# Kernel optimization log

Hardware: AMD Instinct MI355X
Metric: run time of the kernel (lower is better)

Reference implementation:

```python
import jax, jax.numpy as jnp
import numpy as np

N, E, F_IN, H, C = 50000, 800000, 256, 128, 40


def _gcn_norm(edge_index, num_nodes, dtype):
    # add self loops (fill value 1.0), symmetric normalization D^-1/2 A D^-1/2
    src, dst = edge_index[0], edge_index[1]
    loop = jnp.arange(num_nodes, dtype=src.dtype)
    src = jnp.concatenate([src, loop])
    dst = jnp.concatenate([dst, loop])
    w = jnp.ones(src.shape[0], dtype=dtype)
    deg = jax.ops.segment_sum(w, dst, num_segments=num_nodes)
    dinv = jnp.where(deg > 0, jax.lax.rsqrt(deg), jnp.zeros_like(deg))
    norm = dinv[src] * w * dinv[dst]
    return src, dst, norm


def _propagate(x, src, dst, w, num_nodes):
    # gather x[src], scale by edge weight, scatter-add at dst (SpMM)
    return jax.ops.segment_sum(w[:, None] * x[src], dst, num_segments=num_nodes)


def _mixhop_conv(x, src, dst, w, Ws, b):
    # powers = [0, 1, 2]; Ws[p] is [in, out]
    n = x.shape[0]
    outs = [x @ Ws[0]]
    h = x
    for p in (1, 2):
        h = _propagate(h, src, dst, w, n)
        outs.append(h @ Ws[p])
    return jnp.concatenate(outs, axis=-1) + b


def setup_inputs() -> dict:
    key = jax.random.key(0)
    ks = jax.random.split(key, 10)
    x = jax.random.normal(ks[0], (N, F_IN), dtype=jnp.float32)
    edge_index = jax.random.randint(ks[1], (2, E), 0, N, dtype=jnp.int64)
    s1 = 1.0 / np.sqrt(F_IN)
    s2 = 1.0 / np.sqrt(3 * H)
    return {
        "x": x,
        "edge_index": edge_index,
        "W1_0": jax.random.uniform(ks[2], (F_IN, H), jnp.float32, -s1, s1),
        "W1_1": jax.random.uniform(ks[3], (F_IN, H), jnp.float32, -s1, s1),
        "W1_2": jax.random.uniform(ks[4], (F_IN, H), jnp.float32, -s1, s1),
        "b1": jnp.zeros((3 * H,), jnp.float32),
        "W2_0": jax.random.uniform(ks[5], (3 * H, C), jnp.float32, -s2, s2),
        "W2_1": jax.random.uniform(ks[6], (3 * H, C), jnp.float32, -s2, s2),
        "W2_2": jax.random.uniform(ks[7], (3 * H, C), jnp.float32, -s2, s2),
        "b2": jnp.zeros((3 * C,), jnp.float32),
    }


def reference(x, edge_index, W1_0, W1_1, W1_2, b1, W2_0, W2_1, W2_2, b2):
    n = x.shape[0]
    src, dst, w = _gcn_norm(edge_index, n, x.dtype)
    h = jax.nn.relu(_mixhop_conv(x, src, dst, w, (W1_0, W1_1, W1_2), b1))
    # eval mode: dropout is identity
    out = _mixhop_conv(h, src, dst, w, (W2_0, W2_1, W2_2), b2)
    return jax.nn.log_softmax(out, axis=1)
```

## Files before the change

kernel.cpp:

```cpp
#include <hip/hip_runtime.h>
#include <hip/hip_bf16.h>
#include <math.h>

#define N_NODES 50000
#define F_IN 256
#define H1 128
#define C_OUT 40
#define L1W 384
#define L2W 120
#define L2WP 128
#define NBUK 196
#define NBLK1 256

typedef __attribute__((ext_vector_type(8))) short short8;
typedef __attribute__((ext_vector_type(4))) float f32x4;
typedef __attribute__((ext_vector_type(2))) float f32x2;
typedef __attribute__((ext_vector_type(4))) unsigned short us4;

__device__ inline unsigned short f2bf(float f) {
    union { float f; unsigned int u; } x;
    x.f = f;
    unsigned int u = x.u;
    return (unsigned short)((u + 0x7FFF + ((u >> 16) & 1)) >> 16);
}
__device__ inline float bf2f(unsigned short u) {
    union { unsigned int u; float f; } x;
    x.u = (unsigned int)u << 16;
    return x.f;
}
__device__ inline unsigned int pack_fp8x4(float a, float b, float c, float d) {
    int v = 0;
    v = __builtin_amdgcn_cvt_pk_fp8_f32(a, b, v, false);
    v = __builtin_amdgcn_cvt_pk_fp8_f32(c, d, v, true);
    return (unsigned int)v;
}
__device__ inline unsigned char pack_fp8x1(float a) {
    return (unsigned char)(__builtin_amdgcn_cvt_pk_fp8_f32(a, a, 0, false) & 0xFF);
}
#define EDGE_S(r) ((int)((r) & 0xFFFFu))
#define EDGE_W(r) bf2f((unsigned short)((r) >> 16))


__global__ void detect_k(const int* __restrict__ ei, int* __restrict__ flag) {
    __shared__ int any;
    if (threadIdx.x == 0) any = 0;
    __syncthreads();
    int v = 0;
    for (int r = 0; r < 4; r++) {
        int e = threadIdx.x + r * 256;
        v |= ei[e * 2 + 1];
    }
    if (v != 0) atomicOr(&any, 1);
    __syncthreads();
    if (threadIdx.x == 0) *flag = any;
}


__global__ void hist_k(const int* __restrict__ ei, const int* __restrict__ flag,
                       int* __restrict__ cnt, int E) {
    int base = (blockIdx.x * 256 + threadIdx.x) * 4;
    if (base >= E) return;
    if (base + 4 <= E) {
        int d0, d1, d2, d3;
        if (*flag) {
            int4 dv = *(const int4*)(ei + E + base);
            d0 = dv.x; d1 = dv.y; d2 = dv.z; d3 = dv.w;
        } else {
            const long long* e64 = (const long long*)ei;
            longlong2 a = *(const longlong2*)(e64 + E + base);
            longlong2 b = *(const longlong2*)(e64 + E + base + 2);
            d0 = (int)a.x; d1 = (int)a.y; d2 = (int)b.x; d3 = (int)b.y;
        }
        atomicAdd(&cnt[d0], 1);
        atomicAdd(&cnt[d1], 1);
        atomicAdd(&cnt[d2], 1);
        atomicAdd(&cnt[d3], 1);
    } else {
        for (int e = base; e < E; e++) {
            int d = (*flag) ? ei[E + e] : (int)((const long long*)ei)[E + e];
            atomicAdd(&cnt[d], 1);
        }
    }
}


__global__ __launch_bounds__(256) void scan1_k(const int* __restrict__ cnt,
                                               int* __restrict__ bsum, int n) {
    int t = threadIdx.x;
    int i = blockIdx.x * 256 + t;
    int v = (i < n) ? cnt[i] : 0;
    for (int off = 32; off; off >>= 1) v += __shfl_down(v, off, 64);
    __shared__ int ws[4];
    if ((t & 63) == 0) ws[t >> 6] = v;
    __syncthreads();
    if (t == 0) bsum[blockIdx.x] = ws[0] + ws[1] + ws[2] + ws[3];
}

__global__ __launch_bounds__(256) void scan2_k(int* __restrict__ bsum,
                                               int* __restrict__ btot, int nb) {
    __shared__ int s[256];
    int t = threadIdx.x;
    int v = (t < nb) ? bsum[t] : 0;
    s[t] = v;
    __syncthreads();
    for (int off = 1; off < 256; off <<= 1) {
        int u = (t >= off) ? s[t - off] : 0;
        __syncthreads();
        s[t] += u;
        __syncthreads();
    }
    if (t < nb) bsum[t] = s[t] - v;
    if (t == nb - 1) *btot = s[t];
}

__global__ __launch_bounds__(256) void scan3_k(const int* __restrict__ cnt,
                                               const int* __restrict__ bsum,
                                               int* __restrict__ rowptr,
                                               float* __restrict__ dinv, int n) {
    __shared__ int s[256];
    int t = threadIdx.x;
    int i = blockIdx.x * 256 + t;
    int v = (i < n) ? cnt[i] : 0;
    s[t] = v;
    __syncthreads();
    for (int off = 1; off < 256; off <<= 1) {
        int u = (t >= off) ? s[t - off] : 0;
        __syncthreads();
        s[t] += u;
        __syncthreads();
    }
    if (i < n) {
        rowptr[i] = s[t] - v + bsum[blockIdx.x];
        if (dinv) dinv[i] = rsqrtf((float)v + 1.0f);
    }
}


__global__ __launch_bounds__(256) void hist2_k(const int* __restrict__ ei,
                                               const int* __restrict__ flag,
                                               int* __restrict__ cnt2, int E) {
    __shared__ int lcnt[NBUK];
    int t = threadIdx.x, blk = blockIdx.x;
    for (int j = t; j < NBUK; j += 256) lcnt[j] = 0;
    __syncthreads();
    int chunk = (E + NBLK1 - 1) / NBLK1;
    int beg = blk * chunk, end = min(beg + chunk, E);
    bool i32 = (*flag) != 0;
    const long long* e64 = (const long long*)ei;
    for (int e = beg + t; e < end; e += 256) {
        int d = i32 ? ei[E + e] : (int)e64[E + e];
        atomicAdd(&lcnt[d >> 8], 1);
    }
    __syncthreads();
    for (int j = t; j < NBUK; j += 256) cnt2[j * NBLK1 + blk] = lcnt[j];
}

__global__ __launch_bounds__(256) void stage_k(const int* __restrict__ ei,
                                               const int* __restrict__ flag,
                                               const int* __restrict__ off2,
                                               unsigned int* __restrict__ stage, int E) {
    __shared__ int lcur[NBUK];
    int t = threadIdx.x, blk = blockIdx.x;
    for (int j = t; j < NBUK; j += 256) lcur[j] = off2[j * NBLK1 + blk];
    __syncthreads();
    int chunk = (E + NBLK1 - 1) / NBLK1;
    int beg = blk * chunk, end = min(beg + chunk, E);
    bool i32 = (*flag) != 0;
    const long long* e64 = (const long long*)ei;
    for (int e = beg + t; e < end; e += 256) {
        int s, d;
        if (i32) { s = ei[e]; d = ei[E + e]; }
        else { s = (int)e64[e]; d = (int)e64[E + e]; }
        int b = d >> 8;
        int pos = atomicAdd(&lcur[b], 1);
        stage[pos] = ((unsigned int)(d & 255) << 16) | (unsigned int)s;
    }
}

__global__ __launch_bounds__(256) void scatter2_k(const unsigned int* __restrict__ stage,
                                                  const int* __restrict__ off2,
                                                  const int* __restrict__ rowptr,
                                                  const float* __restrict__ dinv,
                                                  unsigned int* __restrict__ csr,
                                                  int E, int n) {
    __shared__ int lfill[256];
    int b = blockIdx.x, t = threadIdx.x;
    int node0 = b << 8;
    int node = node0 + t;
    lfill[t] = (node < n) ? rowptr[node] : 0;
    __syncthreads();
    int segBeg = off2[b * NBLK1];
    int segEnd = (b == NBUK - 1) ? E : off2[(b + 1) * NBLK1];
    for (int e = segBeg + t; e < segEnd; e += 256) {
        unsigned int rec = stage[e];
        int dl = rec >> 16;
        int s = rec & 0xFFFF;
        int d = node0 + dl;
        float w = dinv[s] * dinv[d];
        int pos = atomicAdd(&lfill[dl], 1);
        csr[pos] = ((unsigned int)f2bf(w) << 16) | (unsigned int)s;
    }
}


#define N1PACK ((F_IN / 32) * L1W * 32)
#define N2PACK ((L1W / 32) * L2WP * 32)

__global__ void pack_k(const float* __restrict__ w10, const float* __restrict__ w11,
                       const float* __restrict__ w12, const float* __restrict__ w20,
                       const float* __restrict__ w21, const float* __restrict__ w22,
                       unsigned short* __restrict__ Bp1, unsigned short* __restrict__ Bp2) {
    int idx = blockIdx.x * 256 + threadIdx.x;
    if (idx < N1PACK) {
        int kk = idx & 31;
        int nn = (idx >> 5) % L1W;
        int kt = idx / (L1W * 32);
        int k = kt * 32 + kk;
        int p = nn >> 7, c = nn & 127;
        const float* w = (p == 0) ? w10 : (p == 1) ? w11 : w12;
        Bp1[idx] = f2bf(w[k * H1 + c]);
    } else if (idx < N1PACK + N2PACK) {
        int j = idx - N1PACK;
        int kk = j & 31;
        int nn = (j >> 5) & (L2WP - 1);
        int kt = j >> 12;
        int k = kt * 32 + kk;
        unsigned short v = 0;
        if (nn < L2W) {
            int p = nn / 40, c = nn % 40;
            const float* w = (p == 0) ? w20 : (p == 1) ? w21 : w22;
            v = f2bf(w[k * C_OUT + c]);
        }
        Bp2[j] = v;
    }
}


__global__ __launch_bounds__(256, 3) void mgemm1_k(const float* __restrict__ A,
                                                   const unsigned short* __restrict__ Bp,
                                                   const float* __restrict__ b1,
                                                   unsigned short* __restrict__ Hb,
                                                   unsigned char* __restrict__ Y8, int N) {
    __shared__ unsigned short Bs[2][L1W * 32];
    int tid = threadIdx.x;
    int wave = tid >> 6, lane = tid & 63;
    int m = lane & 15, kq = lane >> 4;
    int row0 = blockIdx.x * 64 + wave * 16;
    int arow = row0 + m;
    if (arow >= N) arow = N - 1;
    const float* Ap = A + (size_t)arow * F_IN + kq * 8;

    f32x4 acc[24];
#pragma unroll
    for (int s = 0; s < 24; s++) acc[s] = (f32x4){0.f, 0.f, 0.f, 0.f};

    short8 breg[6];
    float4 af0, af1;
#pragma unroll
    for (int c = 0; c < 6; c++) {
        int t = tid + c * 256;
        breg[c] = *(const short8*)(Bp + (size_t)t * 8);
    }
    af0 = *(const float4*)(Ap);
    af1 = *(const float4*)(Ap + 4);
#pragma unroll
    for (int c = 0; c < 6; c++) {
        int t = tid + c * 256;
        int col = t >> 2, pp = t & 3;
        *(short8*)(&Bs[0][col * 32 + ((pp ^ ((col >> 1) & 3)) << 3)]) = breg[c];
    }
    __syncthreads();

    for (int kt = 0; kt < F_IN / 32; kt++) {
        short8 a;
        a[0] = (short)f2bf(af0.x); a[1] = (short)f2bf(af0.y);
        a[2] = (short)f2bf(af0.z); a[3] = (short)f2bf(af0.w);
        a[4] = (short)f2bf(af1.x); a[5] = (short)f2bf(af1.y);
        a[6] = (short)f2bf(af1.z); a[7] = (short)f2bf(af1.w);
        if (kt < F_IN / 32 - 1) {
            const unsigned short* Bn = Bp + (size_t)(kt + 1) * L1W * 32;
#pragma unroll
            for (int c = 0; c < 6; c++) {
                int t = tid + c * 256;
                breg[c] = *(const short8*)(Bn + (size_t)t * 8);
            }
            af0 = *(const float4*)(Ap + (kt + 1) * 32);
            af1 = *(const float4*)(Ap + (kt + 1) * 32 + 4);
        }
        const unsigned short* Bbuf = Bs[kt & 1];
#pragma unroll
        for (int s = 0; s < 24; s++) {
            int col = s * 16 + m;
            short8 b = *(const short8*)(&Bbuf[col * 32 + ((kq ^ ((col >> 1) & 3)) << 3)]);
            acc[s] = __builtin_amdgcn_mfma_f32_16x16x32_bf16(a, b, acc[s], 0, 0, 0);
        }
        if (kt < F_IN / 32 - 1) {
            int nb = (kt + 1) & 1;
#pragma unroll
            for (int c = 0; c < 6; c++) {
                int t = tid + c * 256;
                int col = t >> 2, pp = t & 3;
                *(short8*)(&Bs[nb][col * 32 + ((pp ^ ((col >> 1) & 3)) << 3)]) = breg[c];
            }
        }
        __syncthreads();
    }
    int crow = row0 + kq * 4;
#pragma unroll
    for (int s = 0; s < 8; s++) {
        int col = s * 16 + m;
        float bias = b1[col];
#pragma unroll
        for (int r = 0; r < 4; r++) {
            int row = crow + r;
            if (row < N) Hb[(size_t)row * L1W + col] = f2bf(fmaxf(acc[s][r] + bias, 0.f));
        }
    }
#pragma unroll
    for (int r = 0; r < 4; r++) {
        int row = crow + r;
        if (row < N) {
            uint4 u;
            u.x = pack_fp8x4(acc[8][r], acc[9][r], acc[10][r], acc[11][r]);
            u.y = pack_fp8x4(acc[12][r], acc[13][r], acc[14][r], acc[15][r]);
            u.z = pack_fp8x4(acc[16][r], acc[17][r], acc[18][r], acc[19][r]);
            u.w = pack_fp8x4(acc[20][r], acc[21][r], acc[22][r], acc[23][r]);
            *(uint4*)(Y8 + (size_t)row * 256 + m * 16) = u;
        }
    }
}


__global__ __launch_bounds__(256) void mgemm2_k(const unsigned short* __restrict__ A,
                                                const unsigned short* __restrict__ Bp,
                                                unsigned short* __restrict__ Ub,
                                                unsigned char* __restrict__ U8, int N) {
    __shared__ unsigned short Bs[2][L2WP * 32];
    int tid = threadIdx.x;
    int wave = tid >> 6, lane = tid & 63;
    int m = lane & 15, kq = lane >> 4;
    int row0 = blockIdx.x * 64 + wave * 16;
    int arow = row0 + m;
    if (arow >= N) arow = N - 1;
    const unsigned short* Ap = A + (size_t)arow * L1W + kq * 8;

    f32x4 acc[8];
#pragma unroll
    for (int s = 0; s < 8; s++) acc[s] = (f32x4){0.f, 0.f, 0.f, 0.f};

    short8 breg[2];
    short8 areg;
#pragma unroll
    for (int c = 0; c < 2; c++) {
        int t = tid + c * 256;
        breg[c] = *(const short8*)(Bp + (size_t)t * 8);
    }
    areg = *(const short8*)(Ap);
#pragma unroll
    for (int c = 0; c < 2; c++) {
        int t = tid + c * 256;
        int col = t >> 2, pp = t & 3;
        *(short8*)(&Bs[0][col * 32 + ((pp ^ ((col >> 1) & 3)) << 3)]) = breg[c];
    }
    __syncthreads();

    for (int kt = 0; kt < L1W / 32; kt++) {
        short8 a = areg;
        if (kt < L1W / 32 - 1) {
            const unsigned short* Bn = Bp + (size_t)(kt + 1) * L2WP * 32;
#pragma unroll
            for (int c = 0; c < 2; c++) {
                int t = tid + c * 256;
                breg[c] = *(const short8*)(Bn + (size_t)t * 8);
            }
            areg = *(const short8*)(Ap + (kt + 1) * 32);
        }
        const unsigned short* Bbuf = Bs[kt & 1];
#pragma unroll
        for (int s = 0; s < 8; s++) {
            int col = s * 16 + m;
            short8 b = *(const short8*)(&Bbuf[col * 32 + ((kq ^ ((col >> 1) & 3)) << 3)]);
            acc[s] = __builtin_amdgcn_mfma_f32_16x16x32_bf16(a, b, acc[s], 0, 0, 0);
        }
        if (kt < L1W / 32 - 1) {
            int nb = (kt + 1) & 1;
#pragma unroll
            for (int c = 0; c < 2; c++) {
                int t = tid + c * 256;
                int col = t >> 2, pp = t & 3;
                *(short8*)(&Bs[nb][col * 32 + ((pp ^ ((col >> 1) & 3)) << 3)]) = breg[c];
            }
        }
        __syncthreads();
    }
    int crow = row0 + kq * 4;
#pragma unroll
    for (int s = 0; s < 3; s++) {
        int col = s * 16 + m;
#pragma unroll
        for (int r = 0; r < 4; r++) {
            int row = crow + r;
            if (row < N) Ub[(size_t)row * L2WP + col] = f2bf(acc[s][r]);
        }
    }
#pragma unroll
    for (int r = 0; r < 4; r++) {
        int row = crow + r;
        if (row < N) {
            uint2 u;
            u.x = pack_fp8x4(acc[0][r], acc[1][r], acc[2][r], acc[3][r]);
            u.y = pack_fp8x4(acc[4][r], acc[5][r], acc[6][r], acc[7][r]);
            *(uint2*)(U8 + (size_t)row * 128 + m * 8) = u;
        }
    }
}


__global__ __launch_bounds__(256) void prop256f_k(const unsigned char* __restrict__ Y8,
                                                  unsigned short* __restrict__ Hb,
                                                  unsigned char* __restrict__ T8,
                                                  const int* __restrict__ rowptr,
                                                  const unsigned int* __restrict__ csr,
                                                  const float* __restrict__ dinv,
                                                  const float* __restrict__ b1, int n) {
    int wave = threadIdx.x >> 6, lane = threadIdx.x & 63;
    int i = blockIdx.x * 4 + wave;
    if (i >= n) return;
    int beg = rowptr[i], end = rowptr[i + 1];
    float di = dinv[i];
    const unsigned int* sbase = (const unsigned int*)Y8 + lane;
    unsigned int sv = sbase[(size_t)i * 64];
    float w = di * di;
    f32x2 slo = __builtin_amdgcn_cvt_pk_f32_fp8(sv, false);
    f32x2 shi = __builtin_amdgcn_cvt_pk_f32_fp8(sv, true);
    float a0 = w * slo.x, a1 = w * slo.y, a2 = w * shi.x, a3 = w * shi.y;

#define CONS256(rr, vv)                                                       \
    _Pragma("unroll") for (int e = 0; e < 8; e++) {                           \
        float we = EDGE_W(rr[e]);                                             \
        f32x2 lo = __builtin_amdgcn_cvt_pk_f32_fp8(vv[e], false);             \
        f32x2 hi = __builtin_amdgcn_cvt_pk_f32_fp8(vv[e], true);              \
        a0 = fmaf(we, lo.x, a0);                                              \
        a1 = fmaf(we, lo.y, a1);                                              \
        a2 = fmaf(we, hi.x, a2);                                              \
        a3 = fmaf(we, hi.y, a3);                                              \
    }

    int nfull = (end - beg) >> 3;
    unsigned int rrA[8], rrB[8];
    if (nfull > 0) {
#pragma unroll
        for (int e = 0; e < 8; e++) rrA[e] = csr[beg + e];
        int it = 0;
        while (it + 2 <= nfull) {
            {
                unsigned int vv[8];
#pragma unroll
                for (int e = 0; e < 8; e++) vv[e] = sbase[(size_t)EDGE_S(rrA[e]) * 64];
#pragma unroll
                for (int e = 0; e < 8; e++) rrB[e] = csr[beg + ((it + 1) << 3) + e];
                CONS256(rrA, vv)
            }
            {
                unsigned int vv[8];
#pragma unroll
                for (int e = 0; e < 8; e++) vv[e] = sbase[(size_t)EDGE_S(rrB[e]) * 64];
                if (it + 2 < nfull) {
#pragma unroll
                    for (int e = 0; e < 8; e++) rrA[e] = csr[beg + ((it + 2) << 3) + e];
                }
                CONS256(rrB, vv)
            }
            it += 2;
        }
        if (it < nfull) {
            unsigned int vv[8];
#pragma unroll
            for (int e = 0; e < 8; e++) vv[e] = sbase[(size_t)EDGE_S(rrA[e]) * 64];
            CONS256(rrA, vv)
        }
    }
    int k = beg + (nfull << 3);
    if (k < end) {
        unsigned int rrt[8];
#pragma unroll
        for (int e = 0; e < 8; e++) {
            int idx = k + e;
            rrt[e] = csr[idx < end ? idx : beg];
        }
        unsigned int vv[8];
#pragma unroll
        for (int e = 0; e < 8; e++) vv[e] = sbase[(size_t)EDGE_S(rrt[e]) * 64];
#pragma unroll
        for (int e = 0; e < 8; e++) {
            float we = (k + e < end) ? EDGE_W(rrt[e]) : 0.f;
            f32x2 lo = __builtin_amdgcn_cvt_pk_f32_fp8(vv[e], false);
            f32x2 hi = __builtin_amdgcn_cvt_pk_f32_fp8(vv[e], true);
            a0 = fmaf(we, lo.x, a0);
            a1 = fmaf(we, lo.y, a1);
            a2 = fmaf(we, hi.x, a2);
            a3 = fmaf(we, hi.y, a3);
        }
    }
#undef CONS256
    int m = lane >> 2, jj = lane & 3;
    if (jj < 2) {
        float av[4] = {a0, a1, a2, a3};
#pragma unroll
        for (int j = 0; j < 4; j++) {
            int L = (4 * jj + j) * 16 + m;
            Hb[(size_t)i * L1W + 128 + L] = f2bf(fmaxf(av[j] + b1[128 + L], 0.f));
        }
    } else {
        unsigned int o = pack_fp8x4(a0, a1, a2, a3);
        *(unsigned int*)(T8 + (size_t)i * 128 + m * 8 + 4 * (jj - 2)) = o;
    }
}


__global__ __launch_bounds__(256) void prop128f_k(const unsigned char* __restrict__ T8,
                                                  unsigned short* __restrict__ Hb,
                                                  const int* __restrict__ rowptr,
                                                  const unsigned int* __restrict__ csr,
                                                  const float* __restrict__ dinv,
                                                  const float* __restrict__ b1, int n) {
    int wave = threadIdx.x >> 6, lane = threadIdx.x & 63;
    int i = blockIdx.x * 4 + wave;
    if (i >= n) return;
    int beg = rowptr[i], end = rowptr[i + 1];
    float di = dinv[i];
    const unsigned short* sbase = (const unsigned short*)T8 + lane;
    unsigned int sv = sbase[(size_t)i * 64];
    float w = di * di;
    f32x2 sd = __builtin_amdgcn_cvt_pk_f32_fp8(sv, false);
    float a0 = w * sd.x, a1 = w * sd.y;

#define CONS128(rr, vv)                                                       \
    _Pragma("unroll") for (int e = 0; e < 8; e++) {                           \
        float we = EDGE_W(rr[e]);                                             \
        f32x2 d = __builtin_amdgcn_cvt_pk_f32_fp8(vv[e], false);              \
        a0 = fmaf(we, d.x, a0);                                               \
        a1 = fmaf(we, d.y, a1);                                               \
    }

    int nfull = (end - beg) >> 3;
    unsigned int rrA[8], rrB[8];
    if (nfull > 0) {
#pragma unroll
        for (int e = 0; e < 8; e++) rrA[e] = csr[beg + e];
        int it = 0;
        while (it + 2 <= nfull) {
            {
                unsigned int vv[8];
#pragma unroll
                for (int e = 0; e < 8; e++) vv[e] = sbase[(size_t)EDGE_S(rrA[e]) * 64];
#pragma unroll
                for (int e = 0; e < 8; e++) rrB[e] = csr[beg + ((it + 1) << 3) + e];
                CONS128(rrA, vv)
            }
            {
                unsigned int vv[8];
#pragma unroll
                for (int e = 0; e < 8; e++) vv[e] = sbase[(size_t)EDGE_S(rrB[e]) * 64];
                if (it + 2 < nfull) {
#pragma unroll
                    for (int e = 0; e < 8; e++) rrA[e] = csr[beg + ((it + 2) << 3) + e];
                }
                CONS128(rrB, vv)
            }
            it += 2;
        }
        if (it < nfull) {
            unsigned int vv[8];
#pragma unroll
            for (int e = 0; e < 8; e++) vv[e] = sbase[(size_t)EDGE_S(rrA[e]) * 64];
            CONS128(rrA, vv)
        }
    }
    int k = beg + (nfull << 3);
    if (k < end) {
        unsigned int rrt[8];
#pragma unroll
        for (int e = 0; e < 8; e++) {
            int idx = k + e;
            rrt[e] = csr[idx < end ? idx : beg];
        }
        unsigned int vv[8];
#pragma unroll
        for (int e = 0; e < 8; e++) vv[e] = sbase[(size_t)EDGE_S(rrt[e]) * 64];
#pragma unroll
        for (int e = 0; e < 8; e++) {
            float we = (k + e < end) ? EDGE_W(rrt[e]) : 0.f;
            f32x2 d = __builtin_amdgcn_cvt_pk_f32_fp8(vv[e], false);
            a0 = fmaf(we, d.x, a0);
            a1 = fmaf(we, d.y, a1);
        }
    }
#undef CONS128
    int m = lane >> 2, u0 = (2 * lane) & 7;
    int L0 = u0 * 16 + m, L1 = (u0 + 1) * 16 + m;
    Hb[(size_t)i * L1W + 256 + L0] = f2bf(fmaxf(a0 + b1[256 + L0], 0.f));
    Hb[(size_t)i * L1W + 256 + L1] = f2bf(fmaxf(a1 + b1[256 + L1], 0.f));
}


__global__ __launch_bounds__(256) void propU8_k(const unsigned char* __restrict__ U8,
                                                unsigned short* __restrict__ T2a,
                                                unsigned char* __restrict__ T8b,
                                                const int* __restrict__ rowptr,
                                                const unsigned int* __restrict__ csr,
                                                const float* __restrict__ dinv, int n) {
    int wave = threadIdx.x >> 6, lane = threadIdx.x & 63;
    int i = blockIdx.x * 4 + wave;
    if (i >= n) return;
    int beg = rowptr[i], end = rowptr[i + 1];
    float di = dinv[i];
    int g = lane >> 5, c = lane & 31;
    const unsigned int* sbase = (const unsigned int*)U8 + c;
    float a0 = 0.f, a1 = 0.f, a2 = 0.f, a3 = 0.f;
    if (g == 0) {
        unsigned int sv = sbase[(size_t)i * 32];
        float w = di * di;
        f32x2 lo = __builtin_amdgcn_cvt_pk_f32_fp8(sv, false);
        f32x2 hi = __builtin_amdgcn_cvt_pk_f32_fp8(sv, true);
        a0 = w * lo.x; a1 = w * lo.y; a2 = w * hi.x; a3 = w * hi.y;
    }

#define CONSU8(rr, vv)                                                        \
    _Pragma("unroll") for (int j = 0; j < 4; j++) {                           \
        float we = EDGE_W(rr[j]);                                             \
        f32x2 lo = __builtin_amdgcn_cvt_pk_f32_fp8(vv[j], false);             \
        f32x2 hi = __builtin_amdgcn_cvt_pk_f32_fp8(vv[j], true);              \
        a0 = fmaf(we, lo.x, a0);                                              \
        a1 = fmaf(we, lo.y, a1);                                              \
        a2 = fmaf(we, hi.x, a2);                                              \
        a3 = fmaf(we, hi.y, a3);                                              \
    }

    int k0 = beg + g;
    int cnt = (k0 < end) ? ((end - k0 + 1) >> 1) : 0;
    int nfull = cnt >> 2;
    unsigned int rrA[4], rrB[4];
    if (nfull > 0) {
#pragma unroll
        for (int j = 0; j < 4; j++) rrA[j] = csr[k0 + 2 * j];
        int it = 0;
        while (it + 2 <= nfull) {
            {
                unsigned int vv[4];
#pragma unroll
                for (int j = 0; j < 4; j++) vv[j] = sbase[(size_t)EDGE_S(rrA[j]) * 32];
#pragma unroll
                for (int j = 0; j < 4; j++) rrB[j] = csr[k0 + ((it + 1) << 3) + 2 * j];
                CONSU8(rrA, vv)
            }
            {
                unsigned int vv[4];
#pragma unroll
                for (int j = 0; j < 4; j++) vv[j] = sbase[(size_t)EDGE_S(rrB[j]) * 32];
                if (it + 2 < nfull) {
#pragma unroll
                    for (int j = 0; j < 4; j++) rrA[j] = csr[k0 + ((it + 2) << 3) + 2 * j];
                }
                CONSU8(rrB, vv)
            }
            it += 2;
        }
        if (it < nfull) {
            unsigned int vv[4];
#pragma unroll
            for (int j = 0; j < 4; j++) vv[j] = sbase[(size_t)EDGE_S(rrA[j]) * 32];
            CONSU8(rrA, vv)
        }
    }
    int t0 = nfull << 2;
    if (t0 < cnt) {
        unsigned int rrt[4], vv[4];
#pragma unroll
        for (int j = 0; j < 4; j++) {
            int t = t0 + j;
            rrt[j] = csr[t < cnt ? k0 + 2 * t : beg];
        }
#pragma unroll
        for (int j = 0; j < 4; j++) vv[j] = sbase[(size_t)EDGE_S(rrt[j]) * 32];
#pragma unroll
        for (int j = 0; j < 4; j++) {
            float we = (t0 + j < cnt) ? EDGE_W(rrt[j]) : 0.f;
            f32x2 lo = __builtin_amdgcn_cvt_pk_f32_fp8(vv[j], false);
            f32x2 hi = __builtin_amdgcn_cvt_pk_f32_fp8(vv[j], true);
            a0 = fmaf(we, lo.x, a0);
            a1 = fmaf(we, lo.y, a1);
            a2 = fmaf(we, hi.x, a2);
            a3 = fmaf(we, hi.y, a3);
        }
    }
#undef CONSU8
    a0 += __shfl_xor(a0, 32, 64);
    a1 += __shfl_xor(a1, 32, 64);
    a2 += __shfl_xor(a2, 32, 64);
    a3 += __shfl_xor(a3, 32, 64);
    if (lane < 32) {
        int m = lane >> 1, sb = 4 * (lane & 1);
        float av[4] = {a0, a1, a2, a3};
#pragma unroll
        for (int j = 0; j < 4; j++) {
            int L = (sb + j) * 16 + m;
            if (L >= 40 && L < 80) T2a[(size_t)i * 40 + (L - 40)] = f2bf(av[j]);
            else if (L >= 80 && L < 120) T8b[(size_t)i * 40 + (L - 80)] = pack_fp8x1(av[j]);
        }
    }
}


__global__ __launch_bounds__(256) void lsm_prop_k(const unsigned short* __restrict__ Ub,
                                                  const unsigned short* __restrict__ T2a,
                                                  const unsigned char* __restrict__ T8b,
                                                  const int* __restrict__ rowptr,
                                                  const unsigned int* __restrict__ csr,
                                                  const float* __restrict__ dinv,
                                                  const float* __restrict__ b2,
                                                  float* __restrict__ out, int n) {
    int wave = threadIdx.x >> 6;
    int lane = threadIdx.x & 63;
    int i = blockIdx.x * 4 + wave;
    if (i >= n) return;
    int beg = rowptr[i], end = rowptr[i + 1];
    float di = dinv[i];
    int g = lane / 10;
    int c = lane - g * 10;
    bool act = lane < 60;
    const unsigned int* sb = (const unsigned int*)T8b + c;
    float a0 = 0.f, a1 = 0.f, a2 = 0.f, a3 = 0.f;
    if (lane < 10) {
        unsigned int sv = sb[(size_t)i * 10];
        float w = di * di;
        f32x2 lo = __builtin_amdgcn_cvt_pk_f32_fp8(sv, false);
        f32x2 hi = __builtin_amdgcn_cvt_pk_f32_fp8(sv, true);
        a0 = w * lo.x; a1 = w * lo.y; a2 = w * hi.x; a3 = w * hi.y;
    }

#define CONSLS(rr, vv)                                                        \
    _Pragma("unroll") for (int j = 0; j < 4; j++) {                           \
        float we = EDGE_W(rr[j]);                                             \
        f32x2 lo = __builtin_amdgcn_cvt_pk_f32_fp8(vv[j], false);             \
        f32x2 hi = __builtin_amdgcn_cvt_pk_f32_fp8(vv[j], true);              \
        a0 = fmaf(we, lo.x, a0);                                              \
        a1 = fmaf(we, lo.y, a1);                                              \
        a2 = fmaf(we, hi.x, a2);                                              \
        a3 = fmaf(we, hi.y, a3);                                              \
    }

    int k0 = beg + g;
    int cnt = (act && k0 < end) ? ((end - k0 + 5) / 6) : 0;
    int nfull = cnt >> 2;
    unsigned int rrA[4], rrB[4];
    if (nfull > 0) {
#pragma unroll
        for (int j = 0; j < 4; j++) rrA[j] = csr[k0 + 6 * j];
        int it = 0;
        while (it + 2 <= nfull) {
            {
                unsigned int vv[4];
#pragma unroll
                for (int j = 0; j < 4; j++) vv[j] = sb[(size_t)EDGE_S(rrA[j]) * 10];
#pragma unroll
                for (int j = 0; j < 4; j++) rrB[j] = csr[k0 + (it + 1) * 24 + 6 * j];
                CONSLS(rrA, vv)
            }
            {
                unsigned int vv[4];
#pragma unroll
                for (int j = 0; j < 4; j++) vv[j] = sb[(size_t)EDGE_S(rrB[j]) * 10];
                if (it + 2 < nfull) {
#pragma unroll
                    for (int j = 0; j < 4; j++) rrA[j] = csr[k0 + (it + 2) * 24 + 6 * j];
                }
                CONSLS(rrB, vv)
            }
            it += 2;
        }
        if (it < nfull) {
            unsigned int vv[4];
#pragma unroll
            for (int j = 0; j < 4; j++) vv[j] = sb[(size_t)EDGE_S(rrA[j]) * 10];
            CONSLS(rrA, vv)
        }
    }
    int t0 = nfull << 2;
    if (t0 < cnt) {
        unsigned int rrt[4], vv[4];
#pragma unroll
        for (int j = 0; j < 4; j++) {
            int t = t0 + j;
            rrt[j] = csr[t < cnt ? k0 + 6 * t : beg];
        }
#pragma unroll
        for (int j = 0; j < 4; j++) vv[j] = sb[(size_t)EDGE_S(rrt[j]) * 10];
#pragma unroll
        for (int j = 0; j < 4; j++) {
            float we = (t0 + j < cnt) ? EDGE_W(rrt[j]) : 0.f;
            f32x2 lo = __builtin_amdgcn_cvt_pk_f32_fp8(vv[j], false);
            f32x2 hi = __builtin_amdgcn_cvt_pk_f32_fp8(vv[j], true);
            a0 = fmaf(we, lo.x, a0);
            a1 = fmaf(we, lo.y, a1);
            a2 = fmaf(we, hi.x, a2);
            a3 = fmaf(we, hi.y, a3);
        }
    }
#undef CONSLS
    float r0s = a0, r1s = a1, r2s = a2, r3s = a3;
#pragma unroll
    for (int g2 = 1; g2 < 6; g2++) {
        r0s += __shfl(a0, lane + 10 * g2, 64);
        r1s += __shfl(a1, lane + 10 * g2, 64);
        r2s += __shfl(a2, lane + 10 * g2, 64);
        r3s += __shfl(a3, lane + 10 * g2, 64);
    }
    int j1 = lane + 64;
    int idx = j1 - 80;
    int srcl = (idx < 0) ? 0 : (idx >> 2);
    float s0v = __shfl(r0s, srcl, 64);
    float s1v = __shfl(r1s, srcl, 64);
    float s2v = __shfl(r2s, srcl, 64);
    float s3v = __shfl(r3s, srcl, 64);
    int comp = idx & 3;
    float pv = (comp == 0) ? s0v : (comp == 1) ? s1v : (comp == 2) ? s2v : s3v;
    float v0, v1;
    {
        int j = lane;
        float v = (j >= 40) ? bf2f(T2a[(size_t)i * 40 + (j - 40)]) : bf2f(Ub[(size_t)i * L2WP + j]);
        v0 = v + b2[j];
    }
    if (j1 < 120) {
        float v = (j1 < 80) ? bf2f(T2a[(size_t)i * 40 + (j1 - 40)]) : pv;
        v1 = v + b2[j1];
    } else {
        v1 = -INFINITY;
    }
    float m = fmaxf(v0, v1);
    for (int off = 32; off; off >>= 1) m = fmaxf(m, __shfl_xor(m, off, 64));
    float s = expf(v0 - m) + ((j1 < 120) ? expf(v1 - m) : 0.f);
    for (int off = 32; off; off >>= 1) s += __shfl_xor(s, off, 64);
    float ls = logf(s) + m;
    out[(size_t)i * 120 + lane] = v0 - ls;
    if (j1 < 120) out[(size_t)i * 120 + j1] = v1 - ls;
}


static inline size_t align256(size_t x) { return (x + 255) & ~(size_t)255; }

extern "C" void kernel_launch(void* const* d_in, const int* in_sizes, int n_in,
                              void* d_out, int out_size, void* d_ws, size_t ws_size,
                              hipStream_t stream) {
    const float* x = (const float*)d_in[0];
    const int* ei = (const int*)d_in[1];
    const float* W1_0 = (const float*)d_in[2];
    const float* W1_1 = (const float*)d_in[3];
    const float* W1_2 = (const float*)d_in[4];
    const float* b1 = (const float*)d_in[5];
    const float* W2_0 = (const float*)d_in[6];
    const float* W2_1 = (const float*)d_in[7];
    const float* W2_2 = (const float*)d_in[8];
    const float* b2 = (const float*)d_in[9];
    float* out = (float*)d_out;

    const int n = N_NODES;
    const int E = in_sizes[1] / 2;
    const int nb = (n + 255) / 256;
    const int nbe4 = ((E + 3) / 4 + 255) / 256;
    const int n2 = NBUK * NBLK1;
    const int nb2 = (n2 + 255) / 256;

    char* p = (char*)d_ws;
    size_t off = 0;
    auto alloc = [&](size_t bytes) {
        void* r = p + off;
        off = align256(off + bytes);
        return r;
    };
    int* flag = (int*)alloc(4);
    int* cnt = (int*)alloc((size_t)n * 4);
    int* rowptr = (int*)alloc((size_t)(n + 1) * 4);
    int* bsum = (int*)alloc((size_t)nb * 4);
    float* dinv = (float*)alloc((size_t)n * 4);
    unsigned int* csr = (unsigned int*)alloc((size_t)E * 4);
    int* cnt2 = (int*)alloc((size_t)n2 * 4);
    int* off2 = (int*)alloc((size_t)n2 * 4);
    int* bsum2 = (int*)alloc((size_t)nb2 * 4);
    int* tot2 = (int*)alloc(4);
    unsigned int* stage = (unsigned int*)alloc((size_t)E * 4);
    unsigned short* Bp1 = (unsigned short*)alloc((size_t)N1PACK * 2);
    unsigned short* Bp2 = (unsigned short*)alloc((size_t)N2PACK * 2);
    unsigned short* Hb = (unsigned short*)alloc((size_t)n * L1W * 2);
    unsigned char* Y8 = (unsigned char*)alloc((size_t)n * 256);
    unsigned char* T8 = (unsigned char*)alloc((size_t)n * 128);
    unsigned short* Ub = (unsigned short*)alloc((size_t)n * L2WP * 2);
    unsigned char* U8 = (unsigned char*)alloc((size_t)n * 128);
    unsigned short* T2a = (unsigned short*)alloc((size_t)n * C_OUT * 2);
    unsigned char* T8b = (unsigned char*)alloc((size_t)n * C_OUT);
    (void)ws_size;

    detect_k<<<1, 256, 0, stream>>>(ei, flag);

    hipMemsetAsync(cnt, 0, (size_t)n * 4, stream);
    hist_k<<<nbe4, 256, 0, stream>>>(ei, flag, cnt, E);
    scan1_k<<<nb, 256, 0, stream>>>(cnt, bsum, n);
    scan2_k<<<1, 256, 0, stream>>>(bsum, rowptr + n, nb);
    scan3_k<<<nb, 256, 0, stream>>>(cnt, bsum, rowptr, dinv, n);

    hist2_k<<<NBLK1, 256, 0, stream>>>(ei, flag, cnt2, E);
    scan1_k<<<nb2, 256, 0, stream>>>(cnt2, bsum2, n2);
    scan2_k<<<1, 256, 0, stream>>>(bsum2, tot2, nb2);
    scan3_k<<<nb2, 256, 0, stream>>>(cnt2, bsum2, off2, (float*)nullptr, n2);
    stage_k<<<NBLK1, 256, 0, stream>>>(ei, flag, off2, stage, E);
    scatter2_k<<<NBUK, 256, 0, stream>>>(stage, off2, rowptr, dinv, csr, E, n);

    pack_k<<<(N1PACK + N2PACK + 255) / 256, 256, 0, stream>>>(W1_0, W1_1, W1_2,
                                                              W2_0, W2_1, W2_2, Bp1, Bp2);

    mgemm1_k<<<(n + 63) / 64, 256, 0, stream>>>(x, Bp1, b1, Hb, Y8, n);
    prop256f_k<<<(n + 3) / 4, 256, 0, stream>>>(Y8, Hb, T8, rowptr, csr, dinv, b1, n);
    prop128f_k<<<(n + 3) / 4, 256, 0, stream>>>(T8, Hb, rowptr, csr, dinv, b1, n);

    mgemm2_k<<<(n + 63) / 64, 256, 0, stream>>>(Hb, Bp2, Ub, U8, n);
    propU8_k<<<(n + 3) / 4, 256, 0, stream>>>(U8, T2a, T8b, rowptr, csr, dinv, n);

    lsm_prop_k<<<(n + 3) / 4, 256, 0, stream>>>(Ub, T2a, T8b, rowptr, csr, dinv, b2, out, n);
}
```

Before: 346.1 us.

## Split first GEMM across two column halves per row tile

The layer-1 GEMM now launches two blocks per 64-row tile, each computing 192 of the 384 output columns. This halves the accumulator registers and shared memory per block, allowing occupancy to go from 3 to 4 blocks per CU and doubling the grid for more parallelism. The cost is that each block reloads and converts the same fp32 A rows, doubling A reads and conversions. The epilogue is split so each half writes its portion of the bf16 and fp8 outputs.

```diff
diff --git a/kernel.cpp b/kernel.cpp
--- a/kernel.cpp
+++ b/kernel.cpp
@@ -236,35 +236,38 @@
 }
 
 
-__global__ __launch_bounds__(256, 3) void mgemm1_k(const float* __restrict__ A,
+__global__ __launch_bounds__(256, 4) void mgemm1_k(const float* __restrict__ A,
                                                    const unsigned short* __restrict__ Bp,
                                                    const float* __restrict__ b1,
                                                    unsigned short* __restrict__ Hb,
                                                    unsigned char* __restrict__ Y8, int N) {
-    __shared__ unsigned short Bs[2][L1W * 32];
+    __shared__ unsigned short Bs[2][192 * 32];
     int tid = threadIdx.x;
     int wave = tid >> 6, lane = tid & 63;
     int m = lane & 15, kq = lane >> 4;
-    int row0 = blockIdx.x * 64 + wave * 16;
+    int blkM = blockIdx.x >> 1, blkN = blockIdx.x & 1;
+    int s0 = blkN * 12;
+    int row0 = blkM * 64 + wave * 16;
     int arow = row0 + m;
     if (arow >= N) arow = N - 1;
     const float* Ap = A + (size_t)arow * F_IN + kq * 8;
-
-    f32x4 acc[24];
-#pragma unroll
-    for (int s = 0; s < 24; s++) acc[s] = (f32x4){0.f, 0.f, 0.f, 0.f};
-
-    short8 breg[6];
+    const unsigned short* Bp0 = Bp + (size_t)s0 * 16 * 32;
+
+    f32x4 acc[12];
+#pragma unroll
+    for (int s = 0; s < 12; s++) acc[s] = (f32x4){0.f, 0.f, 0.f, 0.f};
+
+    short8 breg[3];
     float4 af0, af1;
 #pragma unroll
-    for (int c = 0; c < 6; c++) {
+    for (int c = 0; c < 3; c++) {
         int t = tid + c * 256;
-        breg[c] = *(const short8*)(Bp + (size_t)t * 8);
+        breg[c] = *(const short8*)(Bp0 + (size_t)t * 8);
     }
     af0 = *(const float4*)(Ap);
     af1 = *(const float4*)(Ap + 4);
 #pragma unroll
-    for (int c = 0; c < 6; c++) {
+    for (int c = 0; c < 3; c++) {
         int t = tid + c * 256;
         int col = t >> 2, pp = t & 3;
         *(short8*)(&Bs[0][col * 32 + ((pp ^ ((col >> 1) & 3)) << 3)]) = breg[c];
@@ -278,9 +281,9 @@
         a[4] = (short)f2bf(af1.x); a[5] = (short)f2bf(af1.y);
         a[6] = (short)f2bf(af1.z); a[7] = (short)f2bf(af1.w);
         if (kt < F_IN / 32 - 1) {
-            const unsigned short* Bn = Bp + (size_t)(kt + 1) * L1W * 32;
-#pragma unroll
-            for (int c = 0; c < 6; c++) {
+            const unsigned short* Bn = Bp0 + (size_t)(kt + 1) * L1W * 32;
+#pragma unroll
+            for (int c = 0; c < 3; c++) {
                 int t = tid + c * 256;
                 breg[c] = *(const short8*)(Bn + (size_t)t * 8);
             }
@@ -289,7 +292,7 @@
         }
         const unsigned short* Bbuf = Bs[kt & 1];
 #pragma unroll
-        for (int s = 0; s < 24; s++) {
+        for (int s = 0; s < 12; s++) {
             int col = s * 16 + m;
             short8 b = *(const short8*)(&Bbuf[col * 32 + ((kq ^ ((col >> 1) & 3)) << 3)]);
             acc[s] = __builtin_amdgcn_mfma_f32_16x16x32_bf16(a, b, acc[s], 0, 0, 0);
@@ -297,7 +300,7 @@
         if (kt < F_IN / 32 - 1) {
             int nb = (kt + 1) & 1;
 #pragma unroll
-            for (int c = 0; c < 6; c++) {
+            for (int c = 0; c < 3; c++) {
                 int t = tid + c * 256;
                 int col = t >> 2, pp = t & 3;
                 *(short8*)(&Bs[nb][col * 32 + ((pp ^ ((col >> 1) & 3)) << 3)]) = breg[c];
@@ -306,26 +309,37 @@
         __syncthreads();
     }
     int crow = row0 + kq * 4;
-#pragma unroll
-    for (int s = 0; s < 8; s++) {
-        int col = s * 16 + m;
-        float bias = b1[col];
+    if (blkN == 0) {
+#pragma unroll
+        for (int s = 0; s < 8; s++) {
+            int col = s * 16 + m;
+            float bias = b1[col];
+#pragma unroll
+            for (int r = 0; r < 4; r++) {
+                int row = crow + r;
+                if (row < N) Hb[(size_t)row * L1W + col] = f2bf(fmaxf(acc[s][r] + bias, 0.f));
+            }
+        }
 #pragma unroll
         for (int r = 0; r < 4; r++) {
             int row = crow + r;
-            if (row < N) Hb[(size_t)row * L1W + col] = f2bf(fmaxf(acc[s][r] + bias, 0.f));
-        }
-    }
-#pragma unroll
-    for (int r = 0; r < 4; r++) {
-        int row = crow + r;
-        if (row < N) {
-            uint4 u;
-            u.x = pack_fp8x4(acc[8][r], acc[9][r], acc[10][r], acc[11][r]);
-            u.y = pack_fp8x4(acc[12][r], acc[13][r], acc[14][r], acc[15][r]);
-            u.z = pack_fp8x4(acc[16][r], acc[17][r], acc[18][r], acc[19][r]);
-            u.w = pack_fp8x4(acc[20][r], acc[21][r], acc[22][r], acc[23][r]);
-            *(uint4*)(Y8 + (size_t)row * 256 + m * 16) = u;
+            if (row < N) {
+                unsigned int u = pack_fp8x4(acc[8][r], acc[9][r], acc[10][r], acc[11][r]);
+                *(unsigned int*)(Y8 + (size_t)row * 256 + m * 16) = u;
+            }
+        }
+    } else {
+#pragma unroll
+        for (int r = 0; r < 4; r++) {
+            int row = crow + r;
+            if (row < N) {
+                unsigned int u0 = pack_fp8x4(acc[0][r], acc[1][r], acc[2][r], acc[3][r]);
+                uint2 u12;
+                u12.x = pack_fp8x4(acc[4][r], acc[5][r], acc[6][r], acc[7][r]);
+                u12.y = pack_fp8x4(acc[8][r], acc[9][r], acc[10][r], acc[11][r]);
+                *(unsigned int*)(Y8 + (size_t)row * 256 + m * 16 + 4) = u0;
+                *(uint2*)(Y8 + (size_t)row * 256 + m * 16 + 8) = u12;
+            }
         }
     }
 }
@@ -918,7 +932,7 @@
     pack_k<<<(N1PACK + N2PACK + 255) / 256, 256, 0, stream>>>(W1_0, W1_1, W1_2,
                                                               W2_0, W2_1, W2_2, Bp1, Bp2);
 
-    mgemm1_k<<<(n + 63) / 64, 256, 0, stream>>>(x, Bp1, b1, Hb, Y8, n);
+    mgemm1_k<<<2 * ((n + 63) / 64), 256, 0, stream>>>(x, Bp1, b1, Hb, Y8, n);
     prop256f_k<<<(n + 3) / 4, 256, 0, stream>>>(Y8, Hb, T8, rowptr, csr, dinv, b1, n);
     prop128f_k<<<(n + 3) / 4, 256, 0, stream>>>(T8, Hb, rowptr, csr, dinv, b1, n);
 
```

Result: no change. 349.0 us (+0.8%).
